# Optimization experiments

Measured on AMD Instinct MI355X. Metric: run time of the kernel, lower is better.

The kernel has to match this reference:

```python
import jax, jax.numpy as jnp
import numpy as np

B, N, D, H, HID = 8, 729, 1152, 12, 4304
HD = D // H
EPS = 1e-6


def _layer_norm(x, g, b):
    mu = jnp.mean(x, axis=-1, keepdims=True)
    var = jnp.mean((x - mu) ** 2, axis=-1, keepdims=True)
    return (x - mu) / jnp.sqrt(var + EPS) * g + b


def setup_inputs() -> dict:
    key = jax.random.key(0)
    ks = jax.random.split(key, 9)
    s = 0.02
    return {
        "x": jax.random.normal(ks[0], (B, N, D), jnp.float32),
        "wq": jax.random.normal(ks[1], (D, D), jnp.float32) * s,
        "bq": jnp.zeros((D,), jnp.float32),
        "wk": jax.random.normal(ks[2], (D, D), jnp.float32) * s,
        "bk": jnp.zeros((D,), jnp.float32),
        "wv": jax.random.normal(ks[3], (D, D), jnp.float32) * s,
        "bv": jnp.zeros((D,), jnp.float32),
        "wo": jax.random.normal(ks[4], (D, D), jnp.float32) * s,
        "bo": jnp.zeros((D,), jnp.float32),
        "ln1_g": jnp.ones((D,), jnp.float32),
        "ln1_b": jnp.zeros((D,), jnp.float32),
        "w_fc1": jax.random.normal(ks[5], (HID, D), jnp.float32) * s,
        "b_fc1": jnp.zeros((HID,), jnp.float32),
        "w_fc2": jax.random.normal(ks[6], (D, HID), jnp.float32) * s,
        "b_fc2": jnp.zeros((D,), jnp.float32),
        "ln2_g": jnp.ones((D,), jnp.float32),
        "ln2_b": jnp.zeros((D,), jnp.float32),
    }


def reference(x, wq, bq, wk, bk, wv, bv, wo, bo, ln1_g, ln1_b,
              w_fc1, b_fc1, w_fc2, b_fc2, ln2_g, ln2_b):
    b, n, d = x.shape
    # split_heads in the source is a plain view (B, H, N, HD) -- NOT a transpose.
    def heads(t):
        return t.reshape(b, H, n, HD)

    Q = heads(x @ wq.T + bq)
    K = heads(x @ wk.T + bk)
    V = heads(x @ wv.T + bv)

    scores = jnp.einsum("bhqd,bhkd->bhqk", Q, K) * (HD ** -0.5)
    attn_w = jax.nn.softmax(scores, axis=-1)
    o = jnp.einsum("bhqk,bhkd->bhqd", attn_w, V)  # [B,H,N,HD]
    o = jnp.swapaxes(o, 1, 2).reshape(b, n, d)
    attn_out = o @ wo.T + bo

    # post-norm: LN(sublayer) + residual
    h = _layer_norm(attn_out, ln1_g, ln1_b) + x

    # quirky MLP: activation applied BEFORE fc1 (faithful to source)
    m = jax.nn.gelu(h, approximate=True)
    m = m @ w_fc1.T + b_fc1
    m = m @ w_fc2.T + b_fc2

    return _layer_norm(m, ln2_g, ln2_b) + h
```

## Files before the change

kernel.cpp:

```cpp
#include <hip/hip_runtime.h>
#include <hip/hip_bf16.h>

#define BF16 __hip_bfloat16

typedef short short8 __attribute__((ext_vector_type(8)));
typedef short short4v __attribute__((ext_vector_type(4)));
typedef float v4f __attribute__((ext_vector_type(4)));
typedef float f4 __attribute__((ext_vector_type(4)));

__device__ float g_bp[1152];
__device__ BF16  g_wm[1152 * 1152];

__device__ __forceinline__ short f2bs(float f) {
    __hip_bfloat16 h = __float2bfloat16(f);
    return *(short*)&h;
}

__device__ __forceinline__ float bs2f(short s) {
    __hip_bfloat16 h = *(__hip_bfloat16*)&s;
    return __bfloat162float(h);
}

__device__ __forceinline__ void async_cp16(const BF16* g, BF16* l) {
    __builtin_amdgcn_global_load_lds(
        (const __attribute__((address_space(1))) void*)g,
        (__attribute__((address_space(3))) void*)l,
        16, 0, 0);
}

__device__ __forceinline__ int xcd_chunk(int u, int nwg) {
    int xcd = u & 7, i = u >> 3;
    int q = nwg >> 3, r = nwg & 7;
    return (xcd < r ? xcd * (q + 1) : r * (q + 1) + (xcd - r) * q) + i;
}

__global__ __launch_bounds__(256) void prep_kernel(
    const float* __restrict__ wq, const float* __restrict__ wk,
    const float* __restrict__ wv, const float* __restrict__ wo,
    const float* __restrict__ wfc1, const float* __restrict__ wfc2,
    const float* __restrict__ x,
    const float* __restrict__ bfc1, const float* __restrict__ bfc2,
    BF16* __restrict__ wbq, BF16* __restrict__ wbk,
    BF16* __restrict__ wbv, BF16* __restrict__ wbo,
    BF16* __restrict__ wbf1t, BF16* __restrict__ wbf2,
    BF16* __restrict__ xb)
{
    __shared__ float tile[64][65];
    const int bid = blockIdx.x;
    const int tid = threadIdx.x;

    if (bid < 16641) {
        const int i = bid * 256 + tid;
        constexpr int N_DD  = 331776;
        constexpr int N4    = 4 * N_DD;
        constexpr int N_F2  = 1253376;
        constexpr int E_F2  = N4 + N_F2;
        constexpr int N_X   = 1679616;
        constexpr int TOTAL = E_F2 + N_X;

        if (i < N4) {
            int seg = i / N_DD, j = i - seg * N_DD;
            const float* s = (seg == 0) ? wq : (seg == 1) ? wk : (seg == 2) ? wv : wo;
            BF16* d = (seg == 0) ? wbq : (seg == 1) ? wbk : (seg == 2) ? wbv : wbo;
            f4 v = ((const f4*)s)[j];
            short4v o = {f2bs(v.x), f2bs(v.y), f2bs(v.z), f2bs(v.w)};
            ((short4v*)d)[j] = o;
        } else if (i < E_F2) {
            int j = i - N4;
            int row = j / 1088;
            int c = (j - row * 1088) * 4;
            short4v o = {0, 0, 0, 0};
            if (c < 4304) {
                f4 v = *(const f4*)(wfc2 + (size_t)row * 4304 + c);
                o[0] = f2bs(v.x); o[1] = f2bs(v.y); o[2] = f2bs(v.z); o[3] = f2bs(v.w);
            }
            *(short4v*)(wbf2 + (size_t)row * 4352 + c) = o;
        } else if (i < TOTAL) {
            int j = i - E_F2;
            f4 v = ((const f4*)x)[j];
            short4v o = {f2bs(v.x), f2bs(v.y), f2bs(v.z), f2bs(v.w)};
            ((short4v*)xb)[j] = o;
        }
    } else if (bid < 17865) {
        const int b2 = bid - 16641;
        const int h0 = (b2 % 68) * 64;
        const int d0 = (b2 / 68) * 64;
#pragma unroll
        for (int i = 0; i < 4; ++i) {
            int lin = tid + i * 256;
            int r = lin >> 4, c4 = lin & 15;
            f4 v = {0.f, 0.f, 0.f, 0.f};
            if (h0 + r < 4304)
                v = *(const f4*)(wfc1 + (size_t)(h0 + r) * 1152 + d0 + c4 * 4);
            tile[r][c4 * 4 + 0] = v.x;
            tile[r][c4 * 4 + 1] = v.y;
            tile[r][c4 * 4 + 2] = v.z;
            tile[r][c4 * 4 + 3] = v.w;
        }
        __syncthreads();
#pragma unroll
        for (int i = 0; i < 2; ++i) {
            int lin = tid + i * 256;
            int dr = lin >> 3, h8 = lin & 7;
            short8 o;
#pragma unroll
            for (int e = 0; e < 8; ++e)
                o[e] = f2bs(tile[h8 * 8 + e][dr]);
            *(short8*)(wbf1t + (size_t)(d0 + dr) * 4352 + h0 + h8 * 8) = o;
        }
    } else {
        const int row = (bid - 17865) * 4 + (tid >> 6);
        const int lane = tid & 63;
        const float* wr = wfc2 + (size_t)row * 4304;
        float s = 0.f;
        for (int k = lane; k < 4304; k += 64) s += wr[k] * bfc1[k];
#pragma unroll
        for (int mm = 1; mm < 64; mm <<= 1) s += __shfl_xor(s, mm, 64);
        if (lane == 0) g_bp[row] = s + bfc2[row];
    }
}

__global__ __launch_bounds__(256) void qkv_wm_kernel(
    const BF16* __restrict__ A,
    const BF16* __restrict__ Wqkv,
    const float* __restrict__ b0, const float* __restrict__ b1,
    const float* __restrict__ b2,
    BF16* __restrict__ C, size_t cstride, int M,
    const BF16* __restrict__ W2,
    const BF16* __restrict__ W1t)
{
    __shared__ __align__(16) BF16 smem[256 * 64];
    const int bid  = blockIdx.x;
    const int tid  = threadIdx.x;
    const int lane = tid & 63;
    const int wave = tid >> 6;
    const int quad = lane >> 4;
    const int l16  = lane & 15;
    const int wm   = (wave >> 1) * 64;
    const int wn   = (wave & 1) * 64;
    const v4f zf = {0.f, 0.f, 0.f, 0.f};
    BF16* As = smem;
    BF16* Bs = smem + 128 * 64;

    v4f acc[4][4];
#pragma unroll
    for (int i = 0; i < 4; ++i)
#pragma unroll
        for (int j = 0; j < 4; ++j) acc[i][j] = zf;

    if (bid < 81) {
        const int m0 = (bid % 9) * 128;
        const int n0 = (bid / 9) * 128;

        const BF16* gA[4]; BF16* lA[4];
        const BF16* gB[4]; BF16* lB[4];
#pragma unroll
        for (int i = 0; i < 4; ++i) {
            int c = tid + i * 256;
            int src = ((((c & 7) - (c >> 3)) & 7) << 3);
            gA[i] = W2 + (size_t)(m0 + (c >> 3)) * 4352 + src;
            gB[i] = W1t + (size_t)(n0 + (c >> 3)) * 4352 + src;
            lA[i] = As + (c & ~63) * 8;
            lB[i] = Bs + (c & ~63) * 8;
        }

        for (int kt = 0; kt < 68; ++kt) {
#pragma unroll
            for (int i = 0; i < 4; ++i) { async_cp16(gA[i], lA[i]); gA[i] += 64; }
#pragma unroll
            for (int i = 0; i < 4; ++i) { async_cp16(gB[i], lB[i]); gB[i] += 64; }
            __syncthreads();
#pragma unroll
            for (int ks = 0; ks < 2; ++ks) {
                short8 af[4], bfg[4];
#pragma unroll
                for (int mt = 0; mt < 4; ++mt) {
                    int row = wm + mt * 16 + l16;
                    af[mt] = *(const short8*)(As + row * 64 + ((((ks << 2) | quad) + row & 7) & 7) * 8);
                }
#pragma unroll
                for (int nt = 0; nt < 4; ++nt) {
                    int row = wn + nt * 16 + l16;
                    bfg[nt] = *(const short8*)(Bs + row * 64 + ((((ks << 2) | quad) + row & 7) & 7) * 8);
                }
#pragma unroll
                for (int mt = 0; mt < 4; ++mt)
#pragma unroll
                    for (int nt = 0; nt < 4; ++nt)
                        acc[mt][nt] = __builtin_amdgcn_mfma_f32_16x16x32_bf16(
                            af[mt], bfg[nt], acc[mt][nt], 0, 0, 0);
            }
            __syncthreads();
        }

#pragma unroll
        for (int mt = 0; mt < 4; ++mt)
#pragma unroll
            for (int nt = 0; nt < 4; ++nt)
#pragma unroll
                for (int r2 = 0; r2 < 4; ++r2) {
                    int row_l = wm + mt * 16 + quad * 4 + r2;
                    int col_l = wn + nt * 16 + l16;
                    smem[row_l * 128 + col_l] = __float2bfloat16(acc[mt][nt][r2]);
                }
        __syncthreads();
#pragma unroll
        for (int p = 0; p < 8; ++p) {
            int idx = p * 256 + tid;
            *(short8*)(g_wm + (size_t)(m0 + (idx >> 4)) * 1152 + n0 + (idx & 15) * 8) =
                *(const short8*)(smem + idx * 8);
        }
    } else {
        const int wg = xcd_chunk(bid - 81, 1242);
        const int m0 = (wg / 27) * 128;
        const int n0 = (wg % 27) * 128;

        const BF16* gA[4]; BF16* lA[4];
        const BF16* gB[4]; BF16* lB[4];
#pragma unroll
        for (int i = 0; i < 4; ++i) {
            int c = tid + i * 256;
            int src = ((((c & 7) - (c >> 3)) & 7) << 3);
            gA[i] = A + (size_t)(m0 + (c >> 3)) * 1152 + src;
            gB[i] = Wqkv + (size_t)(n0 + (c >> 3)) * 1152 + src;
            lA[i] = As + (c & ~63) * 8;
            lB[i] = Bs + (c & ~63) * 8;
        }

        for (int kt = 0; kt < 18; ++kt) {
#pragma unroll
            for (int i = 0; i < 4; ++i) { async_cp16(gA[i], lA[i]); gA[i] += 64; }
#pragma unroll
            for (int i = 0; i < 4; ++i) { async_cp16(gB[i], lB[i]); gB[i] += 64; }
            __syncthreads();
#pragma unroll
            for (int ks = 0; ks < 2; ++ks) {
                short8 af[4], bfg[4];
#pragma unroll
                for (int mt = 0; mt < 4; ++mt) {
                    int row = wm + mt * 16 + l16;
                    af[mt] = *(const short8*)(As + row * 64 + ((((ks << 2) | quad) + row & 7) & 7) * 8);
                }
#pragma unroll
                for (int nt = 0; nt < 4; ++nt) {
                    int row = wn + nt * 16 + l16;
                    bfg[nt] = *(const short8*)(Bs + row * 64 + ((((ks << 2) | quad) + row & 7) & 7) * 8);
                }
#pragma unroll
                for (int mt = 0; mt < 4; ++mt)
#pragma unroll
                    for (int nt = 0; nt < 4; ++nt)
                        acc[mt][nt] = __builtin_amdgcn_mfma_f32_16x16x32_bf16(
                            af[mt], bfg[nt], acc[mt][nt], 0, 0, 0);
            }
            __syncthreads();
        }

        const int sel = n0 / 1152;
        const float* bp = (sel == 0) ? b0 : (sel == 1) ? b1 : b2;
        BF16* Cb = C + (size_t)sel * cstride;
        const int nl0 = n0 - sel * 1152;

        float bv[4];
#pragma unroll
        for (int nt = 0; nt < 4; ++nt)
            bv[nt] = bp[nl0 + wn + nt * 16 + l16];
#pragma unroll
        for (int mt = 0; mt < 4; ++mt)
#pragma unroll
            for (int nt = 0; nt < 4; ++nt)
#pragma unroll
                for (int r2 = 0; r2 < 4; ++r2) {
                    int row_l = wm + mt * 16 + quad * 4 + r2;
                    int col_l = wn + nt * 16 + l16;
                    smem[row_l * 128 + col_l] = __float2bfloat16(acc[mt][nt][r2] + bv[nt]);
                }
        __syncthreads();
#pragma unroll
        for (int p = 0; p < 8; ++p) {
            int idx = p * 256 + tid;
            int row = m0 + (idx >> 4);
            if (row < M)
                *(short8*)(Cb + (size_t)row * 1152 + nl0 + (idx & 15) * 8) =
                    *(const short8*)(smem + idx * 8);
        }
    }
}

__global__ __launch_bounds__(256) void trans_kernel(
    const BF16* __restrict__ V, BF16* __restrict__ VT)
{
    __shared__ __align__(16) BF16 tl[64][128];
    const int bid = blockIdx.x, tid = threadIdx.x;
    const short8 zero8 = {0, 0, 0, 0, 0, 0, 0, 0};

    if (bid < 1152) {
        const int hg = bid / 12, kb = bid - hg * 12;
        const int b = hg / 12, hh = hg - b * 12;
        const BF16* src = V + (size_t)b * 839808 + (size_t)hh * 69984;
        BF16* dst = VT + (size_t)hg * 86016;
        const int kk0 = kb * 64;
#pragma unroll
        for (int i = 0; i < 3; ++i) {
            int c = tid + i * 256;
            int r = c / 12, cg = c - r * 12;
            short8 v = (kk0 + r < 729)
                ? *(const short8*)(src + (size_t)(kk0 + r) * 96 + cg * 8) : zero8;
            *(short8*)(&tl[r][(cg ^ ((r >> 3) & 7)) * 8]) = v;
        }
        __syncthreads();
#pragma unroll
        for (int i = 0; i < 3; ++i) {
            int wc = tid + i * 256;
            int hd = wc >> 3, o = wc & 7;
            int sp = (((hd >> 3) ^ o) << 3) + (hd & 7);
            short8 out;
#pragma unroll
            for (int j = 0; j < 8; ++j)
                out[j] = *(const short*)&tl[o * 8 + j][sp];
            *(short8*)(dst + (size_t)hd * 768 + kk0 + o * 8) = out;
        }
    } else {
        int c = (bid - 1152) * 256 + tid;
        int hg = c / 1536, rem = c - hg * 1536;
        int r = rem / 96, ock = rem - r * 96;
        int kk = ock * 8;
        short8 v = zero8;
        if (r == 0) {
            const short oneb = 0x3F80;
#pragma unroll
            for (int j = 0; j < 8; ++j) v[j] = (kk + j < 729) ? oneb : (short)0;
        }
        *(short8*)(VT + (size_t)hg * 86016 + (size_t)(96 + r) * 768 + kk) = v;
    }
}

template<int TM>
__global__ __launch_bounds__(256) void gemm_bt_t(
    const BF16* __restrict__ A, int lda,
    const BF16* __restrict__ W, int ldb,
    const float* __restrict__ bias, int nbias,
    BF16* __restrict__ C, int ldc,
    int M, int Kr, int nbn)
{
    constexpr int MT = TM / 32;
    __shared__ __align__(16) BF16 smem[(TM + 128) * 64];
    BF16* As = smem;
    BF16* Bs = smem + TM * 64;

    const int tid  = threadIdx.x;
    const int lane = tid & 63;
    const int wave = tid >> 6;
    const int quad = lane >> 4;
    const int l16  = lane & 15;
    const int wm   = (wave >> 1) * (TM / 2);
    const int wn   = (wave & 1) * 64;
    const int wg   = xcd_chunk(blockIdx.x, gridDim.x);
    const int m0   = (wg / nbn) * TM;
    const int n0   = (wg % nbn) * 128;
    if (m0 >= M) return;

    const v4f zf = {0.f, 0.f, 0.f, 0.f};
    v4f acc[MT][4];
#pragma unroll
    for (int i = 0; i < MT; ++i)
#pragma unroll
        for (int j = 0; j < 4; ++j) acc[i][j] = zf;

    const BF16* gA[MT]; BF16* lA[MT];
#pragma unroll
    for (int i = 0; i < MT; ++i) {
        int c = tid + i * 256;
        gA[i] = A + (size_t)(m0 + (c >> 3)) * lda + ((((c & 7) - (c >> 3)) & 7) << 3);
        lA[i] = As + (c & ~63) * 8;
    }
    const BF16* gB[4]; BF16* lB[4];
#pragma unroll
    for (int i = 0; i < 4; ++i) {
        int c = tid + i * 256;
        gB[i] = W + (size_t)(n0 + (c >> 3)) * ldb + ((((c & 7) - (c >> 3)) & 7) << 3);
        lB[i] = Bs + (c & ~63) * 8;
    }

    const int nk = Kr >> 6;
    for (int kt = 0; kt < nk; ++kt) {
#pragma unroll
        for (int i = 0; i < MT; ++i) { async_cp16(gA[i], lA[i]); gA[i] += 64; }
#pragma unroll
        for (int i = 0; i < 4; ++i)  { async_cp16(gB[i], lB[i]); gB[i] += 64; }
        __syncthreads();

#pragma unroll
        for (int ks = 0; ks < 2; ++ks) {
            short8 af[MT], bfg[4];
#pragma unroll
            for (int mt = 0; mt < MT; ++mt) {
                int row = wm + mt * 16 + l16;
                af[mt] = *(const short8*)(As + row * 64 + ((((ks << 2) | quad) + row & 7) & 7) * 8);
            }
#pragma unroll
            for (int nt = 0; nt < 4; ++nt) {
                int row = wn + nt * 16 + l16;
                bfg[nt] = *(const short8*)(Bs + row * 64 + ((((ks << 2) | quad) + row & 7) & 7) * 8);
            }
#pragma unroll
            for (int mt = 0; mt < MT; ++mt)
#pragma unroll
                for (int nt = 0; nt < 4; ++nt)
                    acc[mt][nt] = __builtin_amdgcn_mfma_f32_16x16x32_bf16(
                        af[mt], bfg[nt], acc[mt][nt], 0, 0, 0);
        }
        __syncthreads();
    }

    float bv[4];
#pragma unroll
    for (int nt = 0; nt < 4; ++nt) {
        int col = n0 + wn + nt * 16 + l16;
        bv[nt] = (col < nbias) ? bias[col] : 0.f;
    }
#pragma unroll
    for (int mt = 0; mt < MT; ++mt)
#pragma unroll
        for (int nt = 0; nt < 4; ++nt)
#pragma unroll
            for (int r2 = 0; r2 < 4; ++r2) {
                int row_l = wm + mt * 16 + quad * 4 + r2;
                int col_l = wn + nt * 16 + l16;
                smem[row_l * 128 + col_l] = __float2bfloat16(acc[mt][nt][r2] + bv[nt]);
            }
    __syncthreads();
#pragma unroll
    for (int p = 0; p < TM / 16; ++p) {
        int idx = p * 256 + tid;
        int row = m0 + (idx >> 4);
        if (row < M)
            *(short8*)(C + (size_t)row * ldc + n0 + (idx & 15) * 8) =
                *(const short8*)(smem + idx * 8);
    }
}

__global__ __launch_bounds__(256) void attn_flash3(
    const BF16* __restrict__ Q, const BF16* __restrict__ K,
    const BF16* __restrict__ VT, BF16* __restrict__ O)
{
    constexpr int NQ = 729, HDk = 96, DM = 1152, LDV = 768;
    __shared__ __align__(16) BF16 Ks[64 * 104];
    __shared__ __align__(16) BF16 Vs[112 * 64];
    __shared__ __align__(16) BF16 Ps[4][32 * 64];

    const int id = blockIdx.x;
    const int xcd = id & 7, slot = id >> 3;
    const int hb = slot / 6, qt = slot - hb * 6;
    const int hg = xcd * 12 + hb;
    const int b = hg / 12, hh = hg - b * 12;

    const int tid = threadIdx.x, wave = tid >> 6, lane = tid & 63;
    const int quad = lane >> 4, l16 = lane & 15;
    const size_t kbase = (size_t)b * (NQ * DM) + (size_t)hh * (NQ * HDk);
    const size_t vbase = (size_t)hg * 112 * LDV;

    const short8 zero8 = {0, 0, 0, 0, 0, 0, 0, 0};
    const v4f zf = {0.f, 0.f, 0.f, 0.f};
    const float C2 = 0.14724445f;

    const int q0w = qt * 128 + wave * 32;
    short8 aq[2][3];
#pragma unroll
    for (int mt = 0; mt < 2; ++mt) {
        int qrow = q0w + mt * 16 + l16;
#pragma unroll
        for (int ks = 0; ks < 3; ++ks)
            aq[mt][ks] = (qrow < NQ)
                ? *(const short8*)(Q + kbase + (size_t)qrow * HDk + ks * 32 + quad * 8)
                : zero8;
    }

    int kk_[3], kg_[3];
#pragma unroll
    for (int i = 0; i < 3; ++i) {
        int c = tid + i * 256;
        kk_[i] = c / 12; kg_[i] = c - kk_[i] * 12;
    }
    int vq_[4], vgr_[4], vhd_[4];
#pragma unroll
    for (int i = 0; i < 4; ++i) {
        int q = wave + 4 * i;
        vq_[i] = q;
        int hd = q * 8 + (lane >> 3);
        vhd_[i] = hd;
        vgr_[i] = ((lane & 7) - hd) & 7;
    }

    v4f oacc[2][7];
#pragma unroll
    for (int mt = 0; mt < 2; ++mt)
#pragma unroll
        for (int nt = 0; nt < 7; ++nt) oacc[mt][nt] = zf;

    short8 kreg[3];
#pragma unroll
    for (int i = 0; i < 3; ++i)
        kreg[i] = *(const short8*)(K + kbase + (size_t)kk_[i] * HDk + kg_[i] * 8);

    for (int kt = 0; kt < 12; ++kt) {
        const int k0 = kt * 64;
#pragma unroll
        for (int i = 0; i < 3; ++i)
            *(short8*)(Ks + kk_[i] * 104 + kg_[i] * 8) = kreg[i];
#pragma unroll
        for (int i = 0; i < 4; ++i) {
            if (vq_[i] < 14)
                async_cp16(VT + vbase + (size_t)vhd_[i] * LDV + k0 + vgr_[i] * 8,
                           Vs + vq_[i] * 512);
        }
        asm volatile("s_waitcnt lgkmcnt(0)" ::: "memory");
        __builtin_amdgcn_s_barrier();
        __builtin_amdgcn_sched_barrier(0);
        {
            const int kn = (kt < 11) ? (k0 + 64) : 0;
#pragma unroll
            for (int i = 0; i < 3; ++i)
                kreg[i] = *(const short8*)(K + kbase + (size_t)(kn + kk_[i]) * HDk + kg_[i] * 8);
        }

        v4f s[2][4];
#pragma unroll
        for (int mt = 0; mt < 2; ++mt)
#pragma unroll
            for (int nt = 0; nt < 4; ++nt) s[mt][nt] = zf;
#pragma unroll
        for (int ks = 0; ks < 3; ++ks)
#pragma unroll
            for (int nt = 0; nt < 4; ++nt) {
                short8 bk = *(const short8*)(Ks + (nt * 16 + l16) * 104 + ks * 32 + quad * 8);
#pragma unroll
                for (int mt = 0; mt < 2; ++mt)
                    s[mt][nt] = __builtin_amdgcn_mfma_f32_16x16x32_bf16(
                        aq[mt][ks], bk, s[mt][nt], 0, 0, 0);
            }

        BF16* Pw = &Ps[wave][0];
#pragma unroll
        for (int mt = 0; mt < 2; ++mt)
#pragma unroll
            for (int nt = 0; nt < 4; ++nt)
#pragma unroll
                for (int r = 0; r < 4; ++r)
                    Pw[((mt * 16 + quad * 4 + r) << 6)
                       + ((((nt << 1) | (l16 >> 3)) ^ (quad << 1)) << 3)
                       + (l16 & 7)] =
                        __float2bfloat16(exp2f(s[mt][nt][r] * C2));
        asm volatile("s_waitcnt lgkmcnt(0)" ::: "memory");

        short8 ap[2][2];
#pragma unroll
        for (int mt = 0; mt < 2; ++mt)
#pragma unroll
            for (int kc = 0; kc < 2; ++kc)
                ap[mt][kc] = *(const short8*)(Pw + ((mt * 16 + l16) << 6)
                    + ((((kc << 2) | quad) ^ (((l16 >> 2) & 3) << 1)) << 3));

        asm volatile("s_waitcnt vmcnt(3)" ::: "memory");
        __builtin_amdgcn_s_barrier();
        __builtin_amdgcn_sched_barrier(0);

#pragma unroll
        for (int nt = 0; nt < 7; ++nt) {
            int hd = nt * 16 + l16;
#pragma unroll
            for (int kc = 0; kc < 2; ++kc) {
                short8 bv = *(const short8*)(Vs + hd * 64 + (((kc * 4 + quad) + hd & 7) & 7) * 8);
#pragma unroll
                for (int mt = 0; mt < 2; ++mt)
                    oacc[mt][nt] = __builtin_amdgcn_mfma_f32_16x16x32_bf16(
                        ap[mt][kc], bv, oacc[mt][nt], 0, 0, 0);
            }
        }
        asm volatile("s_waitcnt lgkmcnt(0)" ::: "memory");
        __builtin_amdgcn_s_barrier();
        __builtin_amdgcn_sched_barrier(0);
    }

#pragma unroll
    for (int mt = 0; mt < 2; ++mt) {
        const int qb = q0w + mt * 16 + quad * 4;
#pragma unroll
        for (int r = 0; r < 4; ++r) {
            int q = qb + r;
            float lv = __shfl(oacc[mt][6][r], quad << 4, 64);
            float inv = (lv > 0.f) ? 1.f / lv : 0.f;
            if (q >= NQ) continue;
#pragma unroll
            for (int nt = 0; nt < 6; ++nt)
                O[(size_t)b * (NQ * DM) + (size_t)q * DM + hh * HDk + nt * 16 + l16] =
                    __float2bfloat16(oacc[mt][nt][r] * inv);
        }
    }
}

__device__ __forceinline__ float block_sum256(float v, float* red, int tid)
{
#pragma unroll
    for (int mm = 1; mm < 64; mm <<= 1) v += __shfl_xor(v, mm, 64);
    if ((tid & 63) == 0) red[tid >> 6] = v;
    __syncthreads();
    float r = red[0] + red[1] + red[2] + red[3];
    __syncthreads();
    return r;
}

__global__ __launch_bounds__(256) void ln1_gelu_kernel(
    const BF16* __restrict__ ao, const float* __restrict__ x,
    const float* __restrict__ gw, const float* __restrict__ bw,
    BF16* __restrict__ hout, BF16* __restrict__ gout)
{
    __shared__ float red[4];
    const int row = blockIdx.x, tid = threadIdx.x;
    const bool act = tid < 144;
    float v[8];
    float s = 0.f;
    if (act) {
        short8 pk = ((const short8*)(ao + (size_t)row * 1152))[tid];
#pragma unroll
        for (int j = 0; j < 8; ++j) { v[j] = bs2f(pk[j]); s += v[j]; }
    } else {
#pragma unroll
        for (int j = 0; j < 8; ++j) v[j] = 0.f;
    }
    s = block_sum256(s, red, tid);
    float mu = s * (1.f / 1152.f);
    float vsum = 0.f;
    if (act) {
#pragma unroll
        for (int j = 0; j < 8; ++j) { float d = v[j] - mu; vsum += d * d; }
    }
    vsum = block_sum256(vsum, red, tid);
    float rstd = rsqrtf(vsum * (1.f / 1152.f) + 1e-6f);
    if (act) {
        f4 g0 = ((const f4*)gw)[2 * tid], g1 = ((const f4*)gw)[2 * tid + 1];
        f4 b0 = ((const f4*)bw)[2 * tid], b1 = ((const f4*)bw)[2 * tid + 1];
        const f4* xr = (const f4*)(x + (size_t)row * 1152);
        f4 x0 = xr[2 * tid], x1 = xr[2 * tid + 1];
        short8 ho, go;
#pragma unroll
        for (int j = 0; j < 8; ++j) {
            float gj = (j < 4) ? g0[j] : g1[j - 4];
            float bj = (j < 4) ? b0[j] : b1[j - 4];
            float xj = (j < 4) ? x0[j] : x1[j - 4];
            float hv = (v[j] - mu) * rstd * gj + bj + xj;
            ho[j] = f2bs(hv);
            float t = hv;
            float gl = 0.5f * t * (1.f + tanhf(0.7978845608028654f * (t + 0.044715f * t * t * t)));
            go[j] = f2bs(gl);
        }
        ((short8*)(hout + (size_t)row * 1152))[tid] = ho;
        ((short8*)(gout + (size_t)row * 1152))[tid] = go;
    }
}

__global__ __launch_bounds__(256) void ln2_kernel(
    const BF16* __restrict__ m2, const BF16* __restrict__ hf,
    const float* __restrict__ gw, const float* __restrict__ bw,
    float* __restrict__ out)
{
    __shared__ float red[4];
    const int row = blockIdx.x, tid = threadIdx.x;
    const bool act = tid < 144;
    float v[8];
    float s = 0.f;
    if (act) {
        short8 pk = ((const short8*)(m2 + (size_t)row * 1152))[tid];
#pragma unroll
        for (int j = 0; j < 8; ++j) { v[j] = bs2f(pk[j]); s += v[j]; }
    } else {
#pragma unroll
        for (int j = 0; j < 8; ++j) v[j] = 0.f;
    }
    s = block_sum256(s, red, tid);
    float mu = s * (1.f / 1152.f);
    float vsum = 0.f;
    if (act) {
#pragma unroll
        for (int j = 0; j < 8; ++j) { float d = v[j] - mu; vsum += d * d; }
    }
    vsum = block_sum256(vsum, red, tid);
    float rstd = rsqrtf(vsum * (1.f / 1152.f) + 1e-6f);
    if (act) {
        f4 g0 = ((const f4*)gw)[2 * tid], g1 = ((const f4*)gw)[2 * tid + 1];
        f4 b0 = ((const f4*)bw)[2 * tid], b1 = ((const f4*)bw)[2 * tid + 1];
        short8 hfv = ((const short8*)(hf + (size_t)row * 1152))[tid];
        f4 o0, o1;
#pragma unroll
        for (int j = 0; j < 8; ++j) {
            float gj = (j < 4) ? g0[j] : g1[j - 4];
            float bj = (j < 4) ? b0[j] : b1[j - 4];
            float ov = (v[j] - mu) * rstd * gj + bj + bs2f(hfv[j]);
            if (j < 4) o0[j] = ov; else o1[j - 4] = ov;
        }
        f4* orow = (f4*)(out + (size_t)row * 1152);
        orow[2 * tid] = o0;
        orow[2 * tid + 1] = o1;
    }
}

extern "C" void kernel_launch(void* const* d_in, const int* in_sizes, int n_in,
                              void* d_out, int out_size, void* d_ws, size_t ws_size,
                              hipStream_t stream)
{
    const float* x    = (const float*)d_in[0];
    const float* wq   = (const float*)d_in[1];
    const float* bq   = (const float*)d_in[2];
    const float* wk   = (const float*)d_in[3];
    const float* bk   = (const float*)d_in[4];
    const float* wv   = (const float*)d_in[5];
    const float* bv   = (const float*)d_in[6];
    const float* wo   = (const float*)d_in[7];
    const float* bo   = (const float*)d_in[8];
    const float* ln1g = (const float*)d_in[9];
    const float* ln1b = (const float*)d_in[10];
    const float* wfc1 = (const float*)d_in[11];
    const float* bfc1 = (const float*)d_in[12];
    const float* wfc2 = (const float*)d_in[13];
    const float* bfc2 = (const float*)d_in[14];
    const float* ln2g = (const float*)d_in[15];
    const float* ln2b = (const float*)d_in[16];

    const int T = 8 * 729;
    const int D = 1152, HIDP = 4352;
    const size_t TD = (size_t)T * D;
    const size_t WDD = (size_t)D * D;

    BF16* wbq   = (BF16*)d_ws;
    BF16* wbk   = wbq + WDD;
    BF16* wbv   = wbk + WDD;
    BF16* wbo   = wbv + WDD;
    BF16* wbf1t = wbo + WDD;
    BF16* wbf2  = wbf1t + (size_t)HIDP * D;
    BF16* xb    = wbf2 + (size_t)D * HIDP;
    BF16* S0    = xb + TD;
    BF16* S1    = S0 + TD;
    BF16* S2    = S1 + TD;
    BF16* S3    = S2 + TD;
    BF16* C0    = S3 + TD;
    BF16* C1    = C0 + TD;
    BF16* VT    = C0;

    static float* bp_dev = nullptr;
    static BF16*  wm_dev = nullptr;
    if (!bp_dev) hipGetSymbolAddress((void**)&bp_dev, HIP_SYMBOL(g_bp));
    if (!wm_dev) hipGetSymbolAddress((void**)&wm_dev, HIP_SYMBOL(g_wm));

    dim3 blk(256);

    prep_kernel<<<18153, blk, 0, stream>>>(
        wq, wk, wv, wo, wfc1, wfc2, x, bfc1, bfc2,
        wbq, wbk, wbv, wbo, wbf1t, wbf2, xb);

    qkv_wm_kernel<<<1323, blk, 0, stream>>>(
        xb, wbq, bq, bk, bv, S0, TD, T, wbf2, wbf1t);

    trans_kernel<<<1728, blk, 0, stream>>>(S2, VT);

    attn_flash3<<<576, blk, 0, stream>>>(S0, S1, VT, S3);

    gemm_bt_t<64><<<828, blk, 0, stream>>>(S3, D, wbo, D, bo, D, C0, D, T, D, 9);

    ln1_gelu_kernel<<<T, blk, 0, stream>>>(C0, x, ln1g, ln1b, C1, C0);

    gemm_bt_t<64><<<828, blk, 0, stream>>>(C0, D, wm_dev, D, bp_dev, D, S3, D, T, D, 9);

    ln2_kernel<<<T, blk, 0, stream>>>(S3, C1, ln2g, ln2b, (float*)d_out);
}
```

Baseline: 387.0 us.

## Use 256x256 tiles with 8 waves and double-buffered pipelined loads in QKV GEMM

The fused QKV/weight-merge kernel moves to 512-thread blocks. The QKV part now computes 256x256 output tiles with a double-buffered LDS pipeline that prefetches upcoming K-slices during MFMA work, using manual waitcnt/barrier scheduling and setprio around the MFMAs. This raises arithmetic intensity per LDS load and overlaps global loads with compute. The cost is 128KB of LDS per block and a much larger accumulator register footprint. Tiles can also straddle the Q/K/V boundaries, so the epilogue picks the destination per column and bounds-checks N. The weight-merge branch keeps 128x128 tiles but is split across 8 waves.

```diff
diff --git a/kernel.cpp b/kernel.cpp
--- a/kernel.cpp
+++ b/kernel.cpp
@@ -120,7 +120,7 @@
     }
 }
 
-__global__ __launch_bounds__(256) void qkv_wm_kernel(
+__global__ __launch_bounds__(512, 2) void qkv_wm8_kernel(
     const BF16* __restrict__ A,
     const BF16* __restrict__ Wqkv,
     const float* __restrict__ b0, const float* __restrict__ b1,
@@ -129,62 +129,66 @@
     const BF16* __restrict__ W2,
     const BF16* __restrict__ W1t)
 {
-    __shared__ __align__(16) BF16 smem[256 * 64];
+    __shared__ __align__(16) BF16 smem[65536];
     const int bid  = blockIdx.x;
     const int tid  = threadIdx.x;
     const int lane = tid & 63;
     const int wave = tid >> 6;
     const int quad = lane >> 4;
     const int l16  = lane & 15;
-    const int wm   = (wave >> 1) * 64;
-    const int wn   = (wave & 1) * 64;
     const v4f zf = {0.f, 0.f, 0.f, 0.f};
-    BF16* As = smem;
-    BF16* Bs = smem + 128 * 64;
-
-    v4f acc[4][4];
-#pragma unroll
-    for (int i = 0; i < 4; ++i)
-#pragma unroll
-        for (int j = 0; j < 4; ++j) acc[i][j] = zf;
+
+    int rr[2], sw[2], lo[2];
+#pragma unroll
+    for (int j = 0; j < 2; ++j) {
+        int c = tid + j * 512;
+        rr[j] = c >> 3;
+        sw[j] = (((c & 7) - (c >> 3)) & 7) << 3;
+        lo[j] = (c & ~63) * 8;
+    }
 
     if (bid < 81) {
+        BF16* Am = smem;
+        BF16* Bm = smem + 8192;
         const int m0 = (bid % 9) * 128;
         const int n0 = (bid / 9) * 128;
-
-        const BF16* gA[4]; BF16* lA[4];
-        const BF16* gB[4]; BF16* lB[4];
-#pragma unroll
-        for (int i = 0; i < 4; ++i) {
-            int c = tid + i * 256;
-            int src = ((((c & 7) - (c >> 3)) & 7) << 3);
-            gA[i] = W2 + (size_t)(m0 + (c >> 3)) * 4352 + src;
-            gB[i] = W1t + (size_t)(n0 + (c >> 3)) * 4352 + src;
-            lA[i] = As + (c & ~63) * 8;
-            lB[i] = Bs + (c & ~63) * 8;
+        const int wm = (wave >> 1) * 32;
+        const int wn = (wave & 1) * 64;
+
+        v4f acc[2][4];
+#pragma unroll
+        for (int i = 0; i < 2; ++i)
+#pragma unroll
+            for (int j = 0; j < 4; ++j) acc[i][j] = zf;
+
+        const BF16* gA[2]; const BF16* gB[2];
+#pragma unroll
+        for (int j = 0; j < 2; ++j) {
+            gA[j] = W2 + (size_t)(m0 + rr[j]) * 4352 + sw[j];
+            gB[j] = W1t + (size_t)(n0 + rr[j]) * 4352 + sw[j];
         }
 
         for (int kt = 0; kt < 68; ++kt) {
 #pragma unroll
-            for (int i = 0; i < 4; ++i) { async_cp16(gA[i], lA[i]); gA[i] += 64; }
-#pragma unroll
-            for (int i = 0; i < 4; ++i) { async_cp16(gB[i], lB[i]); gB[i] += 64; }
+            for (int j = 0; j < 2; ++j) { async_cp16(gA[j], Am + lo[j]); gA[j] += 64; }
+#pragma unroll
+            for (int j = 0; j < 2; ++j) { async_cp16(gB[j], Bm + lo[j]); gB[j] += 64; }
             __syncthreads();
 #pragma unroll
             for (int ks = 0; ks < 2; ++ks) {
-                short8 af[4], bfg[4];
-#pragma unroll
-                for (int mt = 0; mt < 4; ++mt) {
+                short8 af[2], bfg[4];
+#pragma unroll
+                for (int mt = 0; mt < 2; ++mt) {
                     int row = wm + mt * 16 + l16;
-                    af[mt] = *(const short8*)(As + row * 64 + ((((ks << 2) | quad) + row & 7) & 7) * 8);
+                    af[mt] = *(const short8*)(Am + row * 64 + ((((ks << 2) | quad) + row & 7) & 7) * 8);
                 }
 #pragma unroll
                 for (int nt = 0; nt < 4; ++nt) {
                     int row = wn + nt * 16 + l16;
-                    bfg[nt] = *(const short8*)(Bs + row * 64 + ((((ks << 2) | quad) + row & 7) & 7) * 8);
+                    bfg[nt] = *(const short8*)(Bm + row * 64 + ((((ks << 2) | quad) + row & 7) & 7) * 8);
                 }
 #pragma unroll
-                for (int mt = 0; mt < 4; ++mt)
+                for (int mt = 0; mt < 2; ++mt)
 #pragma unroll
                     for (int nt = 0; nt < 4; ++nt)
                         acc[mt][nt] = __builtin_amdgcn_mfma_f32_16x16x32_bf16(
@@ -194,7 +198,7 @@
         }
 
 #pragma unroll
-        for (int mt = 0; mt < 4; ++mt)
+        for (int mt = 0; mt < 2; ++mt)
 #pragma unroll
             for (int nt = 0; nt < 4; ++nt)
 #pragma unroll
@@ -205,84 +209,139 @@
                 }
         __syncthreads();
 #pragma unroll
-        for (int p = 0; p < 8; ++p) {
-            int idx = p * 256 + tid;
+        for (int p = 0; p < 4; ++p) {
+            int idx = p * 512 + tid;
             *(short8*)(g_wm + (size_t)(m0 + (idx >> 4)) * 1152 + n0 + (idx & 15) * 8) =
                 *(const short8*)(smem + idx * 8);
         }
     } else {
-        const int wg = xcd_chunk(bid - 81, 1242);
-        const int m0 = (wg / 27) * 128;
-        const int n0 = (wg % 27) * 128;
-
-        const BF16* gA[4]; BF16* lA[4];
-        const BF16* gB[4]; BF16* lB[4];
-#pragma unroll
-        for (int i = 0; i < 4; ++i) {
-            int c = tid + i * 256;
-            int src = ((((c & 7) - (c >> 3)) & 7) << 3);
-            gA[i] = A + (size_t)(m0 + (c >> 3)) * 1152 + src;
-            gB[i] = Wqkv + (size_t)(n0 + (c >> 3)) * 1152 + src;
-            lA[i] = As + (c & ~63) * 8;
-            lB[i] = Bs + (c & ~63) * 8;
-        }
-
-        for (int kt = 0; kt < 18; ++kt) {
-#pragma unroll
-            for (int i = 0; i < 4; ++i) { async_cp16(gA[i], lA[i]); gA[i] += 64; }
-#pragma unroll
-            for (int i = 0; i < 4; ++i) { async_cp16(gB[i], lB[i]); gB[i] += 64; }
-            __syncthreads();
-#pragma unroll
-            for (int ks = 0; ks < 2; ++ks) {
-                short8 af[4], bfg[4];
-#pragma unroll
-                for (int mt = 0; mt < 4; ++mt) {
-                    int row = wm + mt * 16 + l16;
-                    af[mt] = *(const short8*)(As + row * 64 + ((((ks << 2) | quad) + row & 7) & 7) * 8);
+        const int wg = xcd_chunk(bid - 81, 322);
+        const int m0 = (wg / 14) * 256;
+        const int n0 = (wg % 14) * 256;
+        const int wr = wave >> 2;
+        const int wc = wave & 3;
+        BF16* As = smem;
+        BF16* Bs = smem + 32768;
+
+        v4f acc[8][4];
+#pragma unroll
+        for (int i = 0; i < 8; ++i)
+#pragma unroll
+            for (int j = 0; j < 4; ++j) acc[i][j] = zf;
+
+        #define STAGE_A(dd, hh, tt)                                            \
+            {                                                                  \
+                _Pragma("unroll")                                              \
+                for (int j = 0; j < 2; ++j)                                    \
+                    async_cp16(A + (size_t)(m0 + (hh) * 128 + rr[j]) * 1152    \
+                                 + (tt) * 64 + sw[j],                          \
+                               As + (dd) * 16384 + (hh) * 8192 + lo[j]);       \
+            }
+        #define STAGE_B(dd, hh, tt)                                            \
+            {                                                                  \
+                _Pragma("unroll")                                              \
+                for (int j = 0; j < 2; ++j)                                    \
+                    async_cp16(Wqkv + (size_t)(n0 + (hh) * 128 + rr[j]) * 1152 \
+                                 + (tt) * 64 + sw[j],                          \
+                               Bs + (dd) * 16384 + (hh) * 8192 + lo[j]);       \
+            }
+
+        STAGE_B(0, 0, 0); STAGE_B(0, 1, 0);
+        STAGE_A(0, 0, 0); STAGE_A(0, 1, 0);
+        STAGE_B(1, 0, 1); STAGE_B(1, 1, 1);
+        asm volatile("s_waitcnt vmcnt(4)" ::: "memory");
+        __builtin_amdgcn_s_barrier();
+        __builtin_amdgcn_sched_barrier(0);
+
+        short8 bfr[4][2], afr[2][2];
+#pragma unroll 2
+        for (int it = 0; it < 18; ++it) {
+            const int d = it & 1;
+            const BF16* Ad = As + d * 16384;
+            const BF16* Bd = Bs + d * 16384;
+#pragma unroll
+            for (int q = 0; q < 4; ++q) {
+                if (q == 0) {
+#pragma unroll
+                    for (int nt = 0; nt < 4; ++nt) {
+                        int R = wc * 64 + nt * 16 + l16;
+#pragma unroll
+                        for (int ks = 0; ks < 2; ++ks)
+                            bfr[nt][ks] = *(const short8*)(
+                                Bd + R * 64 + ((((ks << 2) | quad) + R & 7) & 7) * 8);
+                    }
                 }
 #pragma unroll
-                for (int nt = 0; nt < 4; ++nt) {
-                    int row = wn + nt * 16 + l16;
-                    bfg[nt] = *(const short8*)(Bs + row * 64 + ((((ks << 2) | quad) + row & 7) & 7) * 8);
+                for (int mi = 0; mi < 2; ++mi) {
+                    int R = wr * 128 + (q * 2 + mi) * 16 + l16;
+#pragma unroll
+                    for (int ks = 0; ks < 2; ++ks)
+                        afr[mi][ks] = *(const short8*)(
+                            Ad + R * 64 + ((((ks << 2) | quad) + R & 7) & 7) * 8);
                 }
-#pragma unroll
-                for (int mt = 0; mt < 4; ++mt)
-#pragma unroll
-                    for (int nt = 0; nt < 4; ++nt)
-                        acc[mt][nt] = __builtin_amdgcn_mfma_f32_16x16x32_bf16(
-                            af[mt], bfg[nt], acc[mt][nt], 0, 0, 0);
-            }
-            __syncthreads();
-        }
-
-        const int sel = n0 / 1152;
-        const float* bp = (sel == 0) ? b0 : (sel == 1) ? b1 : b2;
-        BF16* Cb = C + (size_t)sel * cstride;
-        const int nl0 = n0 - sel * 1152;
+                if (q == 0) { if (it + 1 < 18) STAGE_A(d ^ 1, 0, it + 1); }
+                if (q == 1) { if (it + 1 < 18) STAGE_A(d ^ 1, 1, it + 1); }
+                if (q == 2) { if (it + 2 < 18) STAGE_B(d,     0, it + 2); }
+                if (q == 3) { if (it + 2 < 18) STAGE_B(d,     1, it + 2); }
+
+                __builtin_amdgcn_s_barrier();
+                asm volatile("s_waitcnt lgkmcnt(0)" ::: "memory");
+                __builtin_amdgcn_sched_barrier(0);
+                __builtin_amdgcn_s_setprio(1);
+#pragma unroll
+                for (int ks = 0; ks < 2; ++ks)
+#pragma unroll
+                    for (int mi = 0; mi < 2; ++mi)
+#pragma unroll
+                        for (int nt = 0; nt < 4; ++nt)
+                            acc[q * 2 + mi][nt] = __builtin_amdgcn_mfma_f32_16x16x32_bf16(
+                                afr[mi][ks], bfr[nt][ks], acc[q * 2 + mi][nt], 0, 0, 0);
+                __builtin_amdgcn_s_setprio(0);
+                if (q == 3) {
+                    if (it + 2 < 18)
+                        asm volatile("s_waitcnt vmcnt(4)" ::: "memory");
+                    else
+                        asm volatile("s_waitcnt vmcnt(0)" ::: "memory");
+                }
+                __builtin_amdgcn_s_barrier();
+            }
+        }
+        #undef STAGE_A
+        #undef STAGE_B
 
         float bv[4];
-#pragma unroll
-        for (int nt = 0; nt < 4; ++nt)
-            bv[nt] = bp[nl0 + wn + nt * 16 + l16];
-#pragma unroll
-        for (int mt = 0; mt < 4; ++mt)
+        int csel[4];
+#pragma unroll
+        for (int nt = 0; nt < 4; ++nt) {
+            int col_g = n0 + wc * 64 + nt * 16 + l16;
+            int sel = (col_g >= 2304) ? 2 : (col_g >= 1152) ? 1 : 0;
+            csel[nt] = sel;
+            const float* bp = (sel == 0) ? b0 : (sel == 1) ? b1 : b2;
+            bv[nt] = (col_g < 3456) ? bp[col_g - sel * 1152] : 0.f;
+        }
+#pragma unroll
+        for (int mt = 0; mt < 8; ++mt)
 #pragma unroll
             for (int nt = 0; nt < 4; ++nt)
 #pragma unroll
                 for (int r2 = 0; r2 < 4; ++r2) {
-                    int row_l = wm + mt * 16 + quad * 4 + r2;
-                    int col_l = wn + nt * 16 + l16;
-                    smem[row_l * 128 + col_l] = __float2bfloat16(acc[mt][nt][r2] + bv[nt]);
+                    int row_l = wr * 128 + mt * 16 + quad * 4 + r2;
+                    int col_l = wc * 64 + nt * 16 + l16;
+                    smem[row_l * 256 + col_l] = __float2bfloat16(acc[mt][nt][r2] + bv[nt]);
                 }
+        (void)csel;
         __syncthreads();
 #pragma unroll
-        for (int p = 0; p < 8; ++p) {
-            int idx = p * 256 + tid;
-            int row = m0 + (idx >> 4);
-            if (row < M)
-                *(short8*)(Cb + (size_t)row * 1152 + nl0 + (idx & 15) * 8) =
+        for (int p = 0; p < 16; ++p) {
+            int idx = p * 512 + tid;
+            int row = m0 + (idx >> 5);
+            int col_g = n0 + (idx & 31) * 8;
+            if (row < M && col_g < 3456) {
+                int sel = (col_g >= 2304) ? 2 : (col_g >= 1152) ? 1 : 0;
+                *(short8*)(C + (size_t)sel * cstride + (size_t)row * 1152
+                           + col_g - sel * 1152) =
                     *(const short8*)(smem + idx * 8);
+            }
         }
     }
 }
@@ -757,7 +816,7 @@
         wq, wk, wv, wo, wfc1, wfc2, x, bfc1, bfc2,
         wbq, wbk, wbv, wbo, wbf1t, wbf2, xb);
 
-    qkv_wm_kernel<<<1323, blk, 0, stream>>>(
+    qkv_wm8_kernel<<<403, dim3(512), 0, stream>>>(
         xb, wbq, bq, bk, bv, S0, TD, T, wbf2, wbf1t);
 
     trans_kernel<<<1728, blk, 0, stream>>>(S2, VT);
```

After: 384.6 us. About the same (-0.6%).
